# Optimization experiments

Hardware: AMD Instinct MI355X
Metric: run time of the kernel (lower is better)

## Reference

```python
import jax, jax.numpy as jnp
import numpy as np
import math

B, L, DM, H, ALPHA = 8, 2048, 512, 8, 3
DH = DM // H
SK = min(ALPHA * math.ceil(math.log(L)), L)    # sample_k = U_part = 24
NTOP = min(ALPHA * math.ceil(math.log(L)), L)  # n_top u = 24


def _ln(x, w, b, eps=1e-8):
    # TF-style layernorm (eps inside sqrt), matching custom LayerNorm
    u = x.mean(-1, keepdims=True)
    s = ((x - u) ** 2).mean(-1, keepdims=True)
    return w * (x - u) / jnp.sqrt(s + eps) + b


def setup_inputs() -> dict:
    key = jax.random.key(0)
    ks = jax.random.split(key, 12)
    p = lambda k, shape: jax.random.normal(k, shape, dtype=jnp.float32) * 0.02
    return {
        'queries': jax.random.normal(ks[0], (B, L, DM), dtype=jnp.float32),
        'keys': jax.random.normal(ks[1], (B, L, DM), dtype=jnp.float32),
        'values': jax.random.normal(ks[2], (B, L, DM), dtype=jnp.float32),
        'padding_mask': jnp.ones((B, L), dtype=jnp.float32),
        'Wq': p(ks[3], (DM, DM)), 'bq': jnp.zeros((DM,), jnp.float32),
        'Wk': p(ks[4], (DM, DM)), 'bk': jnp.zeros((DM,), jnp.float32),
        'Wv': p(ks[5], (DM, DM)), 'bv': jnp.zeros((DM,), jnp.float32),
        'Wf': p(ks[6], (DM, DM)), 'bf': jnp.zeros((DM,), jnp.float32),
        'qln_w': jnp.ones((DM,), jnp.float32), 'qln_b': jnp.zeros((DM,), jnp.float32),
        'fln_w': jnp.ones((DM,), jnp.float32), 'fln_b': jnp.zeros((DM,), jnp.float32),
        'index_sample': jax.random.randint(ks[7], (L, SK), 0, L, dtype=jnp.int32),
    }


def reference(queries, keys, values, padding_mask, Wq, bq, Wk, bk, Wv, bv, Wf, bf,
              qln_w, qln_b, fln_w, fln_b, index_sample):
    Bq, Lq, Dm = queries.shape
    Lk = keys.shape[1]
    Dh = Dm // H
    # projections + head split -> (B, H, L, Dh)
    q = (_ln(queries, qln_w, qln_b) @ Wq + bq).reshape(Bq, Lq, H, Dh).transpose(0, 2, 1, 3)
    k = (keys @ Wk + bk).reshape(Bq, Lk, H, Dh).transpose(0, 2, 1, 3)
    v = (values @ Wv + bv).reshape(Bq, Lk, H, Dh).transpose(0, 2, 1, 3)
    # _prob_QK: random K sampling + sparsity measure + top-n_top query selection
    K_sample = k[:, :, index_sample, :]                        # (B,H,Lq,SK,Dh) irregular gather
    QKs = jnp.einsum('bhid,bhijd->bhij', q, K_sample)          # (B,H,Lq,SK)
    M = QKs.max(-1) - QKs.sum(-1) / Lk
    _, m_top = jax.lax.top_k(M, NTOP)                          # (B,H,u)
    q_red = jnp.take_along_axis(q, m_top[..., None], axis=2)   # (B,H,u,Dh)
    # NOTE: source scales by 1/sqrt(full hidden dim D), not head size
    scores = jnp.einsum('bhud,bhkd->bhuk', q_red, k) * (1.0 / math.sqrt(Dm))
    # ProbMask: causal (key <= selected query pos) AND padding at selected queries
    causal = jnp.arange(Lk)[None, None, None, :] <= m_top[..., None]   # (B,H,u,Lk)
    pad_ind = padding_mask[jnp.arange(Bq)[:, None, None], m_top]       # (B,H,u)
    mask = causal & (pad_ind[..., None] != 0)
    scores = jnp.where(mask, scores, -100000.0)
    # initial values = causal cumulative mean of V (with_mask branch)
    v_avg = jnp.cumsum(v, axis=2) / (jnp.cumsum(padding_mask, -1)[:, None, :, None] + 1e-12)
    attn = jax.nn.softmax(scores, axis=-1)
    upd = jnp.einsum('bhuk,bhkd->bhud', attn, v)               # sparse attention output
    bi = jnp.arange(Bq)[:, None, None]
    hi = jnp.arange(H)[None, :, None]
    out = v_avg.at[bi, hi, m_top].set(upd)                     # scatter selected rows back
    out = out.transpose(0, 2, 1, 3).reshape(Bq, Lq, Dm)
    out = out @ Wf + bf
    return _ln(out, fln_w, fln_b)
```

## Files before the change

### kernel.cpp

```cpp
#include <hip/hip_runtime.h>
#include <math.h>

#define L 2048
#define DM 512
#define B_ 8
#define H_ 8
#define DH 64
#define SK 24
#define NTOP 24
#define CHUNK 128
#define NCH (L / CHUNK)
#define VC 32
#define VR 64
#define ABUF 4096

typedef __attribute__((ext_vector_type(8))) short short8;
typedef __attribute__((ext_vector_type(8))) __bf16 bf16x8;
typedef __attribute__((ext_vector_type(4))) float f32x4;

__device__ inline unsigned short f2bf(float x) {
    unsigned u = __float_as_uint(x);
    unsigned r = (u + 0x7FFFu + ((u >> 16) & 1u)) >> 16;
    return (unsigned short)r;
}
__device__ inline float bf2f(unsigned short h) {
    return __uint_as_float(((unsigned)h) << 16);
}

__device__ inline f32x4 MFMA_BF16(short8 a, short8 b, f32x4 c) {
    return __builtin_amdgcn_mfma_f32_16x16x32_bf16(
        __builtin_bit_cast(bf16x8, a), __builtin_bit_cast(bf16x8, b), c, 0, 0, 0);
}

template<bool WANTL>
__device__ inline void cvt8(const float4& x, const float4& y, short8& h, short8& l) {
    float v0 = x.x, v1 = x.y, v2 = x.z, v3 = x.w;
    float v4 = y.x, v5 = y.y, v6 = y.z, v7 = y.w;
    unsigned short h0 = f2bf(v0), h1 = f2bf(v1), h2 = f2bf(v2), h3 = f2bf(v3);
    unsigned short h4 = f2bf(v4), h5 = f2bf(v5), h6 = f2bf(v6), h7 = f2bf(v7);
    h[0] = (short)h0; h[1] = (short)h1; h[2] = (short)h2; h[3] = (short)h3;
    h[4] = (short)h4; h[5] = (short)h5; h[6] = (short)h6; h[7] = (short)h7;
    if (WANTL) {
        l[0] = (short)f2bf(v0 - bf2f(h0)); l[1] = (short)f2bf(v1 - bf2f(h1));
        l[2] = (short)f2bf(v2 - bf2f(h2)); l[3] = (short)f2bf(v3 - bf2f(h3));
        l[4] = (short)f2bf(v4 - bf2f(h4)); l[5] = (short)f2bf(v5 - bf2f(h5));
        l[6] = (short)f2bf(v6 - bf2f(h6)); l[7] = (short)f2bf(v7 - bf2f(h7));
    }
}

__device__ inline int lds_addr(int row, int kblk) {
    return row * 32 + ((kblk ^ ((row >> 1) & 3)) << 3);
}

__device__ inline float waveReduceSum(float v) {
    for (int o = 32; o > 0; o >>= 1) v += __shfl_down(v, o, 64);
    return v;
}
__device__ inline float waveReduceMax(float v) {
    for (int o = 32; o > 0; o >>= 1) v = fmaxf(v, __shfl_down(v, o, 64));
    return v;
}

__global__ __launch_bounds__(256)
void ln_kernel(const float* __restrict__ x, const float* __restrict__ w,
               const float* __restrict__ bvec, float* __restrict__ out) {
    int row = blockIdx.x;
    const float* xr = x + (size_t)row * DM;
    float* orow = out + (size_t)row * DM;
    int tid = threadIdx.x;
    float2 v = *(const float2*)(xr + tid * 2);
    float s = v.x + v.y;
    float sq = v.x * v.x + v.y * v.y;
    __shared__ float red[8];
    float ws = waveReduceSum(s);
    float wq = waveReduceSum(sq);
    int wid = tid >> 6, lane = tid & 63;
    if (lane == 0) { red[wid] = ws; red[4 + wid] = wq; }
    __syncthreads();
    float tot = red[0] + red[1] + red[2] + red[3];
    float totq = red[4] + red[5] + red[6] + red[7];
    float mean = tot * (1.0f / DM);
    float var = totq * (1.0f / DM) - mean * mean;
    float inv = rsqrtf(var + 1e-8f);
    float w0 = w[tid * 2], w1 = w[tid * 2 + 1];
    float b0 = bvec[tid * 2], b1 = bvec[tid * 2 + 1];
    float2 o;
    o.x = w0 * (v.x - mean) * inv + b0;
    o.y = w1 * (v.y - mean) * inv + b1;
    *(float2*)(orow + tid * 2) = o;
}

__global__ __launch_bounds__(256)
void ln_split_kernel(const float* __restrict__ x, const float* __restrict__ w,
                     const float* __restrict__ bvec,
                     unsigned short* __restrict__ oh, unsigned short* __restrict__ ol) {
    int row = blockIdx.x;
    const float* xr = x + (size_t)row * DM;
    int tid = threadIdx.x;
    float2 v = *(const float2*)(xr + tid * 2);
    float s = v.x + v.y;
    float sq = v.x * v.x + v.y * v.y;
    __shared__ float red[8];
    float ws = waveReduceSum(s);
    float wq = waveReduceSum(sq);
    int wid = tid >> 6, lane = tid & 63;
    if (lane == 0) { red[wid] = ws; red[4 + wid] = wq; }
    __syncthreads();
    float tot = red[0] + red[1] + red[2] + red[3];
    float totq = red[4] + red[5] + red[6] + red[7];
    float mean = tot * (1.0f / DM);
    float var = totq * (1.0f / DM) - mean * mean;
    float inv = rsqrtf(var + 1e-8f);
    float w0 = w[tid * 2], w1 = w[tid * 2 + 1];
    float b0 = bvec[tid * 2], b1 = bvec[tid * 2 + 1];
    float o0 = w0 * (v.x - mean) * inv + b0;
    float o1 = w1 * (v.y - mean) * inv + b1;
    ushort2 hh, ll;
    hh.x = f2bf(o0); ll.x = f2bf(o0 - bf2f(hh.x));
    hh.y = f2bf(o1); ll.y = f2bf(o1 - bf2f(hh.y));
    *(ushort2*)(oh + (size_t)row * DM + tid * 2) = hh;
    *(ushort2*)(ol + (size_t)row * DM + tid * 2) = ll;
}

__global__ __launch_bounds__(256)
void wsplit_kernel(const float* __restrict__ W, unsigned short* __restrict__ th,
                   unsigned short* __restrict__ tl) {
    __shared__ float ts[32][33];
    int k0 = blockIdx.y * 32, n0 = blockIdx.x * 32;
    int t = threadIdx.x;
    int r = t >> 3, c = (t & 7) * 4;
    float4 v = *(const float4*)(W + (size_t)(k0 + r) * 512 + n0 + c);
    ts[r][c] = v.x; ts[r][c + 1] = v.y; ts[r][c + 2] = v.z; ts[r][c + 3] = v.w;
    __syncthreads();
    float a0 = ts[c + 0][r], a1 = ts[c + 1][r], a2 = ts[c + 2][r], a3 = ts[c + 3][r];
    ushort4 h, l;
    h.x = f2bf(a0); l.x = f2bf(a0 - bf2f(h.x));
    h.y = f2bf(a1); l.y = f2bf(a1 - bf2f(h.y));
    h.z = f2bf(a2); l.z = f2bf(a2 - bf2f(h.z));
    h.w = f2bf(a3); l.w = f2bf(a3 - bf2f(h.w));
    *(ushort4*)(th + (size_t)(n0 + r) * 512 + k0 + c) = h;
    *(ushort4*)(tl + (size_t)(n0 + r) * 512 + k0 + c) = l;
}

template<int TERMS, int OMODE, int ACVT>
__device__ __forceinline__
void gemm_body(unsigned short* smem,
               const unsigned short* __restrict__ Ah, const unsigned short* __restrict__ Al,
               const float* __restrict__ Af,
               const unsigned short* __restrict__ Bh, const unsigned short* __restrict__ Bl,
               const float* __restrict__ bias, float* __restrict__ C,
               unsigned short* __restrict__ Ch, int orig) {
    unsigned short* sAh = smem;
    unsigned short* sAl = smem + ABUF;
    unsigned short* sBh = smem + (TERMS == 3 ? 2 : 1) * ABUF;
    unsigned short* sBl = sBh + ABUF;

    int j = (orig & 7) * 64 + (orig >> 3);
    int n0 = (j & 3) * 128, m0 = (j >> 2) * 128;

    int tid = threadIdx.x;
    int lane = tid & 63, wv = tid >> 6;
    int wr = wv >> 1, wc = wv & 1;
    int lrow = lane & 15, g = lane >> 4;

    int f0 = tid, f1 = tid + 256;
    int row0 = f0 >> 2, k0b = f0 & 3;
    int row1 = f1 >> 2, k1b = f1 & 3;
    int sa0 = lds_addr(row0, k0b), sa1 = lds_addr(row1, k1b);
    int c0 = k0b * 8, c1 = k1b * 8;

    f32x4 acc[4][4];
#pragma unroll
    for (int mf = 0; mf < 4; mf++)
#pragma unroll
        for (int nf = 0; nf < 4; nf++) acc[mf][nf] = (f32x4){0.f, 0.f, 0.f, 0.f};

    short8 rAh0, rAh1, rAl0, rAl1, rBh0, rBh1, rBl0, rBl1;
    float4 fA00, fA01, fA10, fA11;

    auto LOAD = [&](int kt) {
        int k0 = kt * 32;
        if (ACVT) {
            fA00 = *(const float4*)(Af + (size_t)(m0 + row0) * 512 + k0 + c0);
            fA01 = *(const float4*)(Af + (size_t)(m0 + row0) * 512 + k0 + c0 + 4);
            fA10 = *(const float4*)(Af + (size_t)(m0 + row1) * 512 + k0 + c1);
            fA11 = *(const float4*)(Af + (size_t)(m0 + row1) * 512 + k0 + c1 + 4);
        } else {
            rAh0 = *(const short8*)(Ah + (size_t)(m0 + row0) * 512 + k0 + c0);
            rAh1 = *(const short8*)(Ah + (size_t)(m0 + row1) * 512 + k0 + c1);
            if (TERMS == 3) {
                rAl0 = *(const short8*)(Al + (size_t)(m0 + row0) * 512 + k0 + c0);
                rAl1 = *(const short8*)(Al + (size_t)(m0 + row1) * 512 + k0 + c1);
            }
        }
        rBh0 = *(const short8*)(Bh + (size_t)(n0 + row0) * 512 + k0 + c0);
        rBh1 = *(const short8*)(Bh + (size_t)(n0 + row1) * 512 + k0 + c1);
        if (TERMS >= 2) {
            rBl0 = *(const short8*)(Bl + (size_t)(n0 + row0) * 512 + k0 + c0);
            rBl1 = *(const short8*)(Bl + (size_t)(n0 + row1) * 512 + k0 + c1);
        }
    };
    auto STORE = [&]() {
        if (ACVT) {
            cvt8<TERMS == 3>(fA00, fA01, rAh0, rAl0);
            cvt8<TERMS == 3>(fA10, fA11, rAh1, rAl1);
        }
        *(short8*)&sAh[sa0] = rAh0;
        *(short8*)&sAh[sa1] = rAh1;
        if (TERMS == 3) {
            *(short8*)&sAl[sa0] = rAl0;
            *(short8*)&sAl[sa1] = rAl1;
        }
        *(short8*)&sBh[sa0] = rBh0;
        *(short8*)&sBh[sa1] = rBh1;
        if (TERMS >= 2) {
            *(short8*)&sBl[sa0] = rBl0;
            *(short8*)&sBl[sa1] = rBl1;
        }
    };

    int ra = wr * 64 + lrow;
    int rb = wc * 64 + lrow;
    int abase = ra * 32 + ((g ^ ((ra >> 1) & 3)) << 3);
    int bbase = rb * 32 + ((g ^ ((rb >> 1) & 3)) << 3);

    LOAD(0);
    for (int kt = 0; kt < 16; kt++) {
        STORE();
        __syncthreads();
        if (kt < 15) LOAD(kt + 1);
        short8 ah[4], al[4], bh[4], bl[4];
#pragma unroll
        for (int mf = 0; mf < 4; mf++) {
            ah[mf] = *(const short8*)&sAh[abase + mf * 512];
            if (TERMS == 3) al[mf] = *(const short8*)&sAl[abase + mf * 512];
        }
#pragma unroll
        for (int nf = 0; nf < 4; nf++) {
            bh[nf] = *(const short8*)&sBh[bbase + nf * 512];
            if (TERMS >= 2) bl[nf] = *(const short8*)&sBl[bbase + nf * 512];
        }
#pragma unroll
        for (int mf = 0; mf < 4; mf++)
#pragma unroll
            for (int nf = 0; nf < 4; nf++) {
                acc[mf][nf] = MFMA_BF16(ah[mf], bh[nf], acc[mf][nf]);
                if (TERMS >= 2) acc[mf][nf] = MFMA_BF16(ah[mf], bl[nf], acc[mf][nf]);
                if (TERMS == 3) acc[mf][nf] = MFMA_BF16(al[mf], bh[nf], acc[mf][nf]);
            }
        __syncthreads();
    }

    int crow0 = m0 + wr * 64 + (lane >> 4) * 4;
    int ccol0 = n0 + wc * 64 + lrow;
    float bb[4];
#pragma unroll
    for (int nf = 0; nf < 4; nf++) bb[nf] = bias[ccol0 + nf * 16];
#pragma unroll
    for (int mf = 0; mf < 4; mf++)
#pragma unroll
        for (int nf = 0; nf < 4; nf++)
#pragma unroll
            for (int r = 0; r < 4; r++) {
                float val = acc[mf][nf][r] + bb[nf];
                size_t idx = (size_t)(crow0 + mf * 16 + r) * 512 + ccol0 + nf * 16;
                if (OMODE != 2) C[idx] = val;
                if (OMODE != 0) Ch[idx] = f2bf(val);
            }
}

__global__ __launch_bounds__(256, 2)
void qkv_gemm(const unsigned short* __restrict__ lnq_h, const unsigned short* __restrict__ lnq_l,
              const float* __restrict__ keys, const float* __restrict__ values,
              const unsigned short* __restrict__ wq_h, const unsigned short* __restrict__ wq_l,
              const unsigned short* __restrict__ wk_h, const unsigned short* __restrict__ wk_l,
              const unsigned short* __restrict__ wv_h, const unsigned short* __restrict__ wv_l,
              const float* __restrict__ bq, const float* __restrict__ bk, const float* __restrict__ bv,
              float* __restrict__ qb, float* __restrict__ kb,
              unsigned short* __restrict__ kb_h, unsigned short* __restrict__ vb_h) {
    __shared__ __align__(16) unsigned short smem[4 * ABUF];
    int orig = blockIdx.x + 4 * blockIdx.y;
    if (blockIdx.z == 0)
        gemm_body<3, 0, 0>(smem, lnq_h, lnq_l, nullptr, wq_h, wq_l, bq, qb, nullptr, orig);
    else if (blockIdx.z == 1)
        gemm_body<3, 1, 1>(smem, nullptr, nullptr, keys, wk_h, wk_l, bk, kb, kb_h, orig);
    else
        gemm_body<1, 2, 1>(smem, nullptr, nullptr, values, wv_h, wv_l, bv, nullptr, vb_h, orig);
}

template<int TERMS, int OMODE, int ACVT>
__global__ __launch_bounds__(256, 2)
void gemm_mfma(const unsigned short* __restrict__ Ah, const unsigned short* __restrict__ Al,
               const float* __restrict__ Af,
               const unsigned short* __restrict__ Bh, const unsigned short* __restrict__ Bl,
               const float* __restrict__ bias, float* __restrict__ C,
               unsigned short* __restrict__ Ch) {
    __shared__ __align__(16) unsigned short smem[(TERMS == 3 ? 4 : (TERMS == 2 ? 3 : 2)) * ABUF];
    int orig = blockIdx.x + 4 * blockIdx.y;
    gemm_body<TERMS, OMODE, ACVT>(smem, Ah, Al, Af, Bh, Bl, bias, C, Ch, orig);
}

__global__ __launch_bounds__(256)
void sample_m_kernel(const float* __restrict__ q, const float* __restrict__ k,
                     const int* __restrict__ idx, float* __restrict__ M) {
    int bid = blockIdx.x;
    int b = bid & 7;
    int ig = bid >> 3;
    int wv = threadIdx.x >> 6, lane = threadIdx.x & 63;
    int i = ig * 4 + wv;
    const float* qrow = q + ((size_t)b * L + i) * DM + lane * 8;
    float4 q0 = *(const float4*)qrow;
    float4 q1 = *(const float4*)(qrow + 4);
    int myidx = 0;
    if (lane < SK) myidx = idx[i * SK + lane];
    float sj[SK];
#pragma unroll
    for (int j = 0; j < SK; j++) {
        int row = __shfl(myidx, j, 64);
        const float* kp = k + ((size_t)b * L + row) * DM + lane * 8;
        float4 k0 = *(const float4*)kp;
        float4 k1 = *(const float4*)(kp + 4);
        sj[j] = q0.x * k0.x + q0.y * k0.y + q0.z * k0.z + q0.w * k0.w
              + q1.x * k1.x + q1.y * k1.y + q1.z * k1.z + q1.w * k1.w;
    }
    float mx = -1e30f, sm = 0.f;
#pragma unroll
    for (int j = 0; j < SK; j++) {
        float s = sj[j];
        s += __shfl_xor(s, 1, 64);
        s += __shfl_xor(s, 2, 64);
        s += __shfl_xor(s, 4, 64);
        mx = fmaxf(mx, s);
        sm += s;
    }
    if ((lane & 7) == 0) {
        int h = lane >> 3;
        M[((size_t)b * H_ + h) * L + i] = mx - sm * (1.0f / L);
    }
}

__global__ __launch_bounds__(64)
void topk_kernel(const float* __restrict__ M, int* __restrict__ mtop) {
    int bh = blockIdx.x;
    int lane = threadIdx.x;
    const float* Mr = M + (size_t)bh * L;
    float m[32];
#pragma unroll
    for (int r = 0; r < 32; r++) m[r] = Mr[r * 64 + lane];
    for (int it = 0; it < NTOP; it++) {
        float bv = -1e30f; int br = 0;
#pragma unroll
        for (int r = 0; r < 32; r++) {
            bool better = m[r] > bv;
            br = better ? r : br;
            bv = better ? m[r] : bv;
        }
        int bt = (br << 6) | lane;
#pragma unroll
        for (int o = 1; o < 64; o <<= 1) {
            float ov = __shfl_xor(bv, o, 64);
            int ot = __shfl_xor(bt, o, 64);
            bool take = (ov > bv) || (ov == bv && ot < bt);
            bv = take ? ov : bv;
            bt = take ? ot : bt;
        }
        if (lane == 0) mtop[bh * NTOP + it] = bt;
        int rwin = bt >> 6;
        bool mine = (bt & 63) == lane;
#pragma unroll
        for (int r = 0; r < 32; r++)
            if (mine && (r == rwin)) m[r] = -1e30f;
    }
}

__global__ __launch_bounds__(256)
void qprep_kernel(const float* __restrict__ qb, const int* __restrict__ mtop,
                  const float* __restrict__ pad, unsigned short* __restrict__ qsel,
                  int* __restrict__ lim_arr) {
    int bh = blockIdx.x; int b = bh >> 3, h = bh & 7;
    int tid = threadIdx.x;
#pragma unroll
    for (int l = 0; l < 2; l++) {
        int f = tid + l * 256;
        int u = f >> 4, seg = (f & 15) * 4;
        ushort4 o;
        if (u < NTOP) {
            int iq = mtop[bh * NTOP + u];
            bool ok = pad[(size_t)b * L + iq] != 0.f;
            float sc = ok ? 0.044194173824159216f : 0.f;
            float4 qv = *(const float4*)(qb + ((size_t)b * L + iq) * DM + h * DH + seg);
            o.x = f2bf(qv.x * sc); o.y = f2bf(qv.y * sc);
            o.z = f2bf(qv.z * sc); o.w = f2bf(qv.w * sc);
            if (seg == 0) lim_arr[bh * 32 + u] = ok ? iq : (L - 1);
        } else {
            o.x = o.y = o.z = o.w = 0;
            if (seg == 0) lim_arr[bh * 32 + u] = -1;
        }
        *(ushort4*)(qsel + ((size_t)bh * 32 + u) * 64 + seg) = o;
    }
}

__global__ __launch_bounds__(256)
void padscan_kernel(const float* __restrict__ pad, float* __restrict__ denom) {
    int b = blockIdx.x;
    __shared__ float tot[256];
    int tid = threadIdx.x;
    const float* p = pad + (size_t)b * L;
    float loc[8];
    float s = 0.f;
#pragma unroll
    for (int u = 0; u < 8; u++) { s += p[tid * 8 + u]; loc[u] = s; }
    tot[tid] = s;
    __syncthreads();
    for (int off = 1; off < 256; off <<= 1) {
        float add = (tid >= off) ? tot[tid - off] : 0.f;
        __syncthreads();
        tot[tid] += add;
        __syncthreads();
    }
    float excl = tot[tid] - s;
#pragma unroll
    for (int u = 0; u < 8; u++) denom[(size_t)b * L + tid * 8 + u] = excl + loc[u];
}

__global__ __launch_bounds__(256)
void vsum_kernel(const unsigned short* __restrict__ vh, float* __restrict__ csum) {
    int c = blockIdx.x, b = blockIdx.y;
    int d2 = threadIdx.x;
    size_t base = ((size_t)b * L + c * VR) * DM + d2 * 2;
    float a0 = 0.f, a1 = 0.f;
    for (int t = 0; t < VR; t++) {
        unsigned v = *(const unsigned*)(vh + base + (size_t)t * DM);
        a0 += bf2f((unsigned short)(v & 0xffff));
        a1 += bf2f((unsigned short)(v >> 16));
    }
    float2 st = {a0, a1};
    *(float2*)(csum + ((size_t)b * VC + c) * DM + d2 * 2) = st;
}

__global__ __launch_bounds__(256)
void vavg_kernel(const unsigned short* __restrict__ vh, const float* __restrict__ csum,
                 const float* __restrict__ denom, unsigned short* __restrict__ out_h) {
    int c = blockIdx.x, b = blockIdx.y;
    int d2 = threadIdx.x;
    float a0 = 0.f, a1 = 0.f;
    for (int cc = 0; cc < c; cc++) {
        float2 t = *(const float2*)(csum + ((size_t)b * VC + cc) * DM + d2 * 2);
        a0 += t.x; a1 += t.y;
    }
    size_t base = ((size_t)b * L + c * VR) * DM + d2 * 2;
    for (int t = 0; t < VR; t++) {
        unsigned v = *(const unsigned*)(vh + base + (size_t)t * DM);
        a0 += bf2f((unsigned short)(v & 0xffff));
        a1 += bf2f((unsigned short)(v >> 16));
        float dn = denom[(size_t)b * L + c * VR + t] + 1e-12f;
        unsigned o = (unsigned)f2bf(a0 / dn) | ((unsigned)f2bf(a1 / dn) << 16);
        *(unsigned*)(out_h + base + (size_t)t * DM) = o;
    }
}

__global__ __launch_bounds__(256)
void attn_chunk_mfma(const unsigned short* __restrict__ kbh,
                     const unsigned short* __restrict__ vbh,
                     const unsigned short* __restrict__ qsel,
                     const int* __restrict__ lim_arr,
                     float* __restrict__ part_m, float* __restrict__ part_s,
                     float* __restrict__ part_acc) {
    int c = blockIdx.x, bh = blockIdx.y;
    int b = bh >> 3, h = bh & 7;
    int j0 = c * CHUNK;
    __shared__ __align__(16) unsigned short KV[128 * 64];
    __shared__ __align__(16) unsigned short Ps[32 * 128];
    __shared__ __align__(16) unsigned short Qs[32 * 64];
    __shared__ float redm[4][32];
    __shared__ float reds[4][32];
    __shared__ int lims[32];

    int tid = threadIdx.x;
    int wv = tid >> 6, lane = tid & 63;
    int l15 = lane & 15, g = lane >> 4;

    const unsigned short* kpanel = kbh + ((size_t)b * L + j0) * DM + h * DH;
    short8 kreg[4];
#pragma unroll
    for (int l = 0; l < 4; l++) {
        int f = tid + l * 256;
        int jr = f >> 3, blk = f & 7;
        kreg[l] = *(const short8*)(kpanel + (size_t)jr * DM + blk * 8);
    }
    {
        int u = tid >> 3, blk = tid & 7;
        short8 qreg = *(const short8*)(qsel + ((size_t)bh * 32 + u) * 64 + blk * 8);
        *(short8*)&Qs[u * 64 + (((blk ^ (u & 7))) << 3)] = qreg;
    }
#pragma unroll
    for (int l = 0; l < 4; l++) {
        int f = tid + l * 256;
        int jr = f >> 3, blk = f & 7;
        *(short8*)&KV[jr * 64 + ((blk ^ (jr & 7)) << 3)] = kreg[l];
    }
    if (tid < 32) lims[tid] = lim_arr[bh * 32 + tid];
    __syncthreads();

    f32x4 sf[2][2];
#pragma unroll
    for (int mf = 0; mf < 2; mf++)
#pragma unroll
        for (int nf = 0; nf < 2; nf++) sf[mf][nf] = (f32x4){0.f, 0.f, 0.f, 0.f};
#pragma unroll
    for (int ks = 0; ks < 2; ks++) {
        short8 aq[2], bk[2];
#pragma unroll
        for (int mf = 0; mf < 2; mf++) {
            int u = mf * 16 + l15;
            int blk = (ks * 4 + g) ^ (u & 7);
            aq[mf] = *(const short8*)&Qs[u * 64 + (blk << 3)];
        }
#pragma unroll
        for (int nf = 0; nf < 2; nf++) {
            int jr = wv * 32 + nf * 16 + l15;
            int blk = (ks * 4 + g) ^ (jr & 7);
            bk[nf] = *(const short8*)&KV[jr * 64 + (blk << 3)];
        }
#pragma unroll
        for (int mf = 0; mf < 2; mf++)
#pragma unroll
            for (int nf = 0; nf < 2; nf++)
                sf[mf][nf] = MFMA_BF16(aq[mf], bk[nf], sf[mf][nf]);
    }

    const unsigned short* vpanel = vbh + ((size_t)b * L + j0) * DM + h * DH;
    short8 vreg[4];
#pragma unroll
    for (int l = 0; l < 4; l++) {
        int f = tid + l * 256;
        int jr = f >> 3, blk = f & 7;
        vreg[l] = *(const short8*)(vpanel + (size_t)jr * DM + blk * 8);
    }

    float sv[2][2][4];
    float mx[2][4];
#pragma unroll
    for (int mf = 0; mf < 2; mf++)
#pragma unroll
        for (int r = 0; r < 4; r++) {
            int u = mf * 16 + g * 4 + r;
            int limv = lims[u];
            float m = -1e30f;
#pragma unroll
            for (int nf = 0; nf < 2; nf++) {
                int jg = j0 + wv * 32 + nf * 16 + l15;
                float s = (jg <= limv) ? sf[mf][nf][r] : -1e30f;
                sv[mf][nf][r] = s;
                m = fmaxf(m, s);
            }
            m = fmaxf(m, __shfl_xor(m, 1, 64));
            m = fmaxf(m, __shfl_xor(m, 2, 64));
            m = fmaxf(m, __shfl_xor(m, 4, 64));
            m = fmaxf(m, __shfl_xor(m, 8, 64));
            mx[mf][r] = m;
        }
    if (l15 == 0) {
#pragma unroll
        for (int mf = 0; mf < 2; mf++)
#pragma unroll
            for (int r = 0; r < 4; r++)
                redm[wv][mf * 16 + g * 4 + r] = mx[mf][r];
    }
    __syncthreads();

    float lmax[2][4], smv[2][4];
#pragma unroll
    for (int mf = 0; mf < 2; mf++)
#pragma unroll
        for (int r = 0; r < 4; r++) {
            int u = mf * 16 + g * 4 + r;
            float m = fmaxf(fmaxf(redm[0][u], redm[1][u]),
                            fmaxf(redm[2][u], redm[3][u]));
            lmax[mf][r] = m;
            bool any = m > -1e29f;
            float sm = 0.f;
#pragma unroll
            for (int nf = 0; nf < 2; nf++) {
                float e = any ? __expf(sv[mf][nf][r] - m) : 0.f;
                sm += e;
                int jr = wv * 32 + nf * 16 + l15;
                Ps[u * 128 + (((jr >> 3) ^ (u & 7)) << 3) + (jr & 7)] = f2bf(e);
            }
            sm += __shfl_xor(sm, 1, 64);
            sm += __shfl_xor(sm, 2, 64);
            sm += __shfl_xor(sm, 4, 64);
            sm += __shfl_xor(sm, 8, 64);
            smv[mf][r] = sm;
        }
    if (l15 == 0) {
#pragma unroll
        for (int mf = 0; mf < 2; mf++)
#pragma unroll
            for (int r = 0; r < 4; r++)
                reds[wv][mf * 16 + g * 4 + r] = smv[mf][r];
    }
#pragma unroll
    for (int l = 0; l < 4; l++) {
        int f = tid + l * 256;
        int jr = f >> 3, blk = f & 7;
        short8 w = vreg[l];
        if ((jr >> 3) & 1) w = __builtin_shufflevector(w, w, 4, 5, 6, 7, 0, 1, 2, 3);
        *(short8*)&KV[jr * 64 + ((blk ^ (jr & 7)) << 3)] = w;
    }
    __syncthreads();

    if (wv == 0 && l15 == 0) {
#pragma unroll
        for (int mf = 0; mf < 2; mf++)
#pragma unroll
            for (int r = 0; r < 4; r++) {
                int u = mf * 16 + g * 4 + r;
                if (u < NTOP) {
                    float ss = reds[0][u] + reds[1][u] + reds[2][u] + reds[3][u];
                    part_m[(bh * NTOP + u) * NCH + c] = lmax[mf][r];
                    part_s[(bh * NTOP + u) * NCH + c] = ss;
                }
            }
    }

    f32x4 of[2];
    of[0] = (f32x4){0.f, 0.f, 0.f, 0.f};
    of[1] = (f32x4){0.f, 0.f, 0.f, 0.f};
    int d = wv * 16 + l15;
#pragma unroll
    for (int ks = 0; ks < 4; ks++) {
        unsigned short va[8];
#pragma unroll
        for (int i = 0; i < 8; i++) {
            int jr = ks * 32 + g * 8 + i;
            int addr = jr * 64 + (((d >> 3) ^ (jr & 7)) << 3)
                     + ((d & 7) ^ (((jr >> 3) & 1) << 2));
            va[i] = KV[addr];
        }
        short8 av;
#pragma unroll
        for (int i = 0; i < 8; i++) av[i] = (short)va[i];
        short8 bp[2];
#pragma unroll
        for (int nf = 0; nf < 2; nf++) {
            int u = nf * 16 + l15;
            int blk = (ks * 4 + g) ^ (u & 7);
            bp[nf] = *(const short8*)&Ps[u * 128 + (blk << 3)];
        }
#pragma unroll
        for (int nf = 0; nf < 2; nf++)
            of[nf] = MFMA_BF16(av, bp[nf], of[nf]);
    }
#pragma unroll
    for (int nf = 0; nf < 2; nf++) {
        int u = nf * 16 + l15;
        if (u < NTOP) {
#pragma unroll
            for (int r = 0; r < 4; r++)
                part_acc[((size_t)(bh * NTOP + u) * NCH + c) * 64 + wv * 16 + g * 4 + r] =
                    of[nf][r];
        }
    }
}

__global__ __launch_bounds__(256)
void attn_merge_kernel(const float* __restrict__ part_m, const float* __restrict__ part_s,
                       const float* __restrict__ part_acc, const int* __restrict__ mtop,
                       unsigned short* __restrict__ pre_h) {
    int ug = blockIdx.x;
    int bh = blockIdx.y;
    int b = bh >> 3, h = bh & 7;
    int tid = threadIdx.x;
    int u = ug * 4 + (tid >> 6);
    int d = tid & 63;
    int base = (bh * NTOP + u) * NCH;
    float m = -1e30f;
#pragma unroll
    for (int c = 0; c < NCH; c++) m = fmaxf(m, part_m[base + c]);
    float s = 0.f, o = 0.f;
#pragma unroll
    for (int c = 0; c < NCH; c++) {
        float w = __expf(part_m[base + c] - m);
        s += part_s[base + c] * w;
        o = fmaf(part_acc[(size_t)(base + c) * 64 + d], w, o);
    }
    o /= s;
    int iq = mtop[bh * NTOP + u];
    pre_h[((size_t)b * L + iq) * DM + h * DH + d] = f2bf(o);
}

extern "C" void kernel_launch(void* const* d_in, const int* in_sizes, int n_in,
                              void* d_out, int out_size, void* d_ws, size_t ws_size,
                              hipStream_t stream) {
    const float* queries = (const float*)d_in[0];
    const float* keys    = (const float*)d_in[1];
    const float* values  = (const float*)d_in[2];
    const float* pad     = (const float*)d_in[3];
    const float* Wq = (const float*)d_in[4];  const float* bq = (const float*)d_in[5];
    const float* Wk = (const float*)d_in[6];  const float* bk = (const float*)d_in[7];
    const float* Wv = (const float*)d_in[8];  const float* bv = (const float*)d_in[9];
    const float* Wf = (const float*)d_in[10]; const float* bfv = (const float*)d_in[11];
    const float* qlnw = (const float*)d_in[12]; const float* qlnb = (const float*)d_in[13];
    const float* flnw = (const float*)d_in[14]; const float* flnb = (const float*)d_in[15];
    const int* idx = (const int*)d_in[16];

    float* ws = (float*)d_ws;
    const size_t NE = (size_t)B_ * L * DM;
    float* qb    = ws;
    float* kb    = ws + NE;
    unsigned short* vb_h = (unsigned short*)(ws + 2 * NE);
    unsigned short* kb_h = vb_h + NE;
    unsigned short* qsel = (unsigned short*)(ws + 3 * NE);
    int* lim_arr = (int*)(qsel + 64 * 32 * 64);
    float* Mbuf  = ws + 4 * NE;
    float* denom = Mbuf + (size_t)B_ * H_ * L;
    float* csum  = denom + (size_t)B_ * L;
    int*   mtop  = (int*)(csum + (size_t)B_ * VC * DM);
    unsigned short* bfr = (unsigned short*)(mtop + 2048);
    unsigned short* pre_h = bfr;
    unsigned short* wts   = bfr + NE;
    unsigned short* wq_h = wts;              unsigned short* wq_l = wts + 262144;
    unsigned short* wk_h = wts + 2 * 262144; unsigned short* wk_l = wts + 3 * 262144;
    unsigned short* wv_h = wts + 4 * 262144; unsigned short* wv_l = wts + 5 * 262144;
    unsigned short* wf_h = wts + 6 * 262144; unsigned short* wf_l = wts + 7 * 262144;

    float* tmp = (float*)d_out;
    unsigned short* lnq_h = (unsigned short*)d_out;
    unsigned short* lnq_l = lnq_h + NE;
    float* part_m   = tmp;
    float* part_s   = part_m + 64 * NTOP * NCH;
    float* part_acc = part_s + 64 * NTOP * NCH;

    padscan_kernel<<<B_, 256, 0, stream>>>(pad, denom);
    ln_split_kernel<<<B_ * L, 256, 0, stream>>>(queries, qlnw, qlnb, lnq_h, lnq_l);
    dim3 gw(16, 16);
    wsplit_kernel<<<gw, 256, 0, stream>>>(Wq, wq_h, wq_l);
    wsplit_kernel<<<gw, 256, 0, stream>>>(Wk, wk_h, wk_l);
    wsplit_kernel<<<gw, 256, 0, stream>>>(Wv, wv_h, wv_l);
    wsplit_kernel<<<gw, 256, 0, stream>>>(Wf, wf_h, wf_l);

    dim3 gq(4, 128, 3);
    qkv_gemm<<<gq, 256, 0, stream>>>(lnq_h, lnq_l, keys, values,
                                     wq_h, wq_l, wk_h, wk_l, wv_h, wv_l,
                                     bq, bk, bv, qb, kb, kb_h, vb_h);

    sample_m_kernel<<<B_ * L / 4, 256, 0, stream>>>(qb, kb, idx, Mbuf);
    topk_kernel<<<B_ * H_, 64, 0, stream>>>(Mbuf, mtop);
    qprep_kernel<<<64, 256, 0, stream>>>(qb, mtop, pad, qsel, lim_arr);
    dim3 gv(VC, B_);
    vsum_kernel<<<gv, 256, 0, stream>>>(vb_h, csum);
    vavg_kernel<<<gv, 256, 0, stream>>>(vb_h, csum, denom, pre_h);
    dim3 gc(NCH, 64);
    attn_chunk_mfma<<<gc, 256, 0, stream>>>(kb_h, vb_h, qsel, lim_arr,
                                            part_m, part_s, part_acc);
    dim3 gmg(6, 64);
    attn_merge_kernel<<<gmg, 256, 0, stream>>>(part_m, part_s, part_acc, mtop, pre_h);
    dim3 gg(4, 128);
    gemm_mfma<1, 0, 0><<<gg, 256, 0, stream>>>(pre_h, nullptr, nullptr, wf_h, wf_l, bfv, (float*)d_out, nullptr);
    ln_kernel<<<B_ * L, 256, 0, stream>>>((float*)d_out, flnw, flnb, (float*)d_out);
}
```

Before: 242.3 us.

## Load GEMM B tiles directly into LDS with double buffering

Moves the B-operand (weight) tile loads from a register staging path to global_load_lds direct-to-LDS transfers. The B tiles are double-buffered so the next tile streams in while the current one is consumed, and the XOR swizzle is applied on the source address. This cuts register pressure and the VGPR-to-LDS store instructions, at the cost of more LDS per block. The larger LDS footprint may reduce occupancy, and the asynchronous loads depend on correct waitcnt/barrier ordering.

New measurement: 254.8 us. +5.2%, slower.

```diff
diff --git a/kernel.cpp b/kernel.cpp
--- a/kernel.cpp
+++ b/kernel.cpp
@@ -30,6 +30,12 @@
 __device__ inline f32x4 MFMA_BF16(short8 a, short8 b, f32x4 c) {
     return __builtin_amdgcn_mfma_f32_16x16x32_bf16(
         __builtin_bit_cast(bf16x8, a), __builtin_bit_cast(bf16x8, b), c, 0, 0, 0);
+}
+
+__device__ __forceinline__ void gload16(const unsigned short* g, unsigned short* l) {
+    __builtin_amdgcn_global_load_lds(
+        (const __attribute__((address_space(1))) void*)g,
+        (__attribute__((address_space(3))) void*)l, 16, 0, 0);
 }
 
 template<bool WANTL>
@@ -150,10 +156,11 @@
                const unsigned short* __restrict__ Bh, const unsigned short* __restrict__ Bl,
                const float* __restrict__ bias, float* __restrict__ C,
                unsigned short* __restrict__ Ch, int orig) {
+    constexpr int A_ARR = (TERMS == 3) ? 2 : 1;
+    constexpr int B_ARR = (TERMS >= 2) ? 2 : 1;
     unsigned short* sAh = smem;
     unsigned short* sAl = smem + ABUF;
-    unsigned short* sBh = smem + (TERMS == 3 ? 2 : 1) * ABUF;
-    unsigned short* sBl = sBh + ABUF;
+    unsigned short* sB  = smem + A_ARR * ABUF;
 
     int j = (orig & 7) * 64 + (orig >> 3);
     int n0 = (j & 3) * 128, m0 = (j >> 2) * 128;
@@ -163,11 +170,10 @@
     int wr = wv >> 1, wc = wv & 1;
     int lrow = lane & 15, g = lane >> 4;
 
-    int f0 = tid, f1 = tid + 256;
-    int row0 = f0 >> 2, k0b = f0 & 3;
-    int row1 = f1 >> 2, k1b = f1 & 3;
-    int sa0 = lds_addr(row0, k0b), sa1 = lds_addr(row1, k1b);
-    int c0 = k0b * 8, c1 = k1b * 8;
+    int row0 = tid >> 2, k0b = tid & 3;
+    int row1 = row0 + 64;
+    int sa0 = lds_addr(row0, k0b), sa1 = lds_addr(row1, k0b);
+    int c0 = k0b * 8;
 
     f32x4 acc[4][4];
 #pragma unroll
@@ -175,32 +181,26 @@
 #pragma unroll
         for (int nf = 0; nf < 4; nf++) acc[mf][nf] = (f32x4){0.f, 0.f, 0.f, 0.f};
 
-    short8 rAh0, rAh1, rAl0, rAl1, rBh0, rBh1, rBl0, rBl1;
+    short8 rAh0, rAh1, rAl0, rAl1;
     float4 fA00, fA01, fA10, fA11;
 
-    auto LOAD = [&](int kt) {
+    auto LOAD_A = [&](int kt) {
         int k0 = kt * 32;
         if (ACVT) {
             fA00 = *(const float4*)(Af + (size_t)(m0 + row0) * 512 + k0 + c0);
             fA01 = *(const float4*)(Af + (size_t)(m0 + row0) * 512 + k0 + c0 + 4);
-            fA10 = *(const float4*)(Af + (size_t)(m0 + row1) * 512 + k0 + c1);
-            fA11 = *(const float4*)(Af + (size_t)(m0 + row1) * 512 + k0 + c1 + 4);
+            fA10 = *(const float4*)(Af + (size_t)(m0 + row1) * 512 + k0 + c0);
+            fA11 = *(const float4*)(Af + (size_t)(m0 + row1) * 512 + k0 + c0 + 4);
         } else {
             rAh0 = *(const short8*)(Ah + (size_t)(m0 + row0) * 512 + k0 + c0);
-            rAh1 = *(const short8*)(Ah + (size_t)(m0 + row1) * 512 + k0 + c1);
+            rAh1 = *(const short8*)(Ah + (size_t)(m0 + row1) * 512 + k0 + c0);
             if (TERMS == 3) {
                 rAl0 = *(const short8*)(Al + (size_t)(m0 + row0) * 512 + k0 + c0);
-                rAl1 = *(const short8*)(Al + (size_t)(m0 + row1) * 512 + k0 + c1);
+                rAl1 = *(const short8*)(Al + (size_t)(m0 + row1) * 512 + k0 + c0);
             }
         }
-        rBh0 = *(const short8*)(Bh + (size_t)(n0 + row0) * 512 + k0 + c0);
-        rBh1 = *(const short8*)(Bh + (size_t)(n0 + row1) * 512 + k0 + c1);
-        if (TERMS >= 2) {
-            rBl0 = *(const short8*)(Bl + (size_t)(n0 + row0) * 512 + k0 + c0);
-            rBl1 = *(const short8*)(Bl + (size_t)(n0 + row1) * 512 + k0 + c1);
-        }
     };
-    auto STORE = [&]() {
+    auto STORE_A = [&]() {
         if (ACVT) {
             cvt8<TERMS == 3>(fA00, fA01, rAh0, rAl0);
             cvt8<TERMS == 3>(fA10, fA11, rAh1, rAl1);
@@ -211,11 +211,21 @@
             *(short8*)&sAl[sa0] = rAl0;
             *(short8*)&sAl[sa1] = rAl1;
         }
-        *(short8*)&sBh[sa0] = rBh0;
-        *(short8*)&sBh[sa1] = rBh1;
+    };
+    auto GLOAD_B = [&](int kt, int buf) {
+        int k0 = kt * 32;
+        int r0 = wv * 16 + (lane >> 2);
+        int kpos = lane & 3;
+        int src0 = (kpos ^ ((r0 >> 1) & 3)) * 8;
+        int r1 = r0 + 64;
+        int src1 = (kpos ^ ((r1 >> 1) & 3)) * 8;
+        unsigned short* bh = sB + (buf * B_ARR + 0) * ABUF;
+        gload16(Bh + (size_t)(n0 + r0) * 512 + k0 + src0, bh + wv * 512);
+        gload16(Bh + (size_t)(n0 + r1) * 512 + k0 + src1, bh + 2048 + wv * 512);
         if (TERMS >= 2) {
-            *(short8*)&sBl[sa0] = rBl0;
-            *(short8*)&sBl[sa1] = rBl1;
+            unsigned short* bl = sB + (buf * B_ARR + 1) * ABUF;
+            gload16(Bl + (size_t)(n0 + r0) * 512 + k0 + src0, bl + wv * 512);
+            gload16(Bl + (size_t)(n0 + r1) * 512 + k0 + src1, bl + 2048 + wv * 512);
         }
     };
 
@@ -224,11 +234,14 @@
     int abase = ra * 32 + ((g ^ ((ra >> 1) & 3)) << 3);
     int bbase = rb * 32 + ((g ^ ((rb >> 1) & 3)) << 3);
 
-    LOAD(0);
+    LOAD_A(0);
+    GLOAD_B(0, 0);
     for (int kt = 0; kt < 16; kt++) {
-        STORE();
+        STORE_A();
         __syncthreads();
-        if (kt < 15) LOAD(kt + 1);
+        if (kt < 15) { GLOAD_B(kt + 1, (kt + 1) & 1); LOAD_A(kt + 1); }
+        const unsigned short* bhB = sB + ((kt & 1) * B_ARR + 0) * ABUF;
+        const unsigned short* blB = sB + ((kt & 1) * B_ARR + 1) * ABUF;
         short8 ah[4], al[4], bh[4], bl[4];
 #pragma unroll
         for (int mf = 0; mf < 4; mf++) {
@@ -237,8 +250,8 @@
         }
 #pragma unroll
         for (int nf = 0; nf < 4; nf++) {
-            bh[nf] = *(const short8*)&sBh[bbase + nf * 512];
-            if (TERMS >= 2) bl[nf] = *(const short8*)&sBl[bbase + nf * 512];
+            bh[nf] = *(const short8*)&bhB[bbase + nf * 512];
+            if (TERMS >= 2) bl[nf] = *(const short8*)&blB[bbase + nf * 512];
         }
 #pragma unroll
         for (int mf = 0; mf < 4; mf++)
@@ -278,7 +291,7 @@
               const float* __restrict__ bq, const float* __restrict__ bk, const float* __restrict__ bv,
               float* __restrict__ qb, float* __restrict__ kb,
               unsigned short* __restrict__ kb_h, unsigned short* __restrict__ vb_h) {
-    __shared__ __align__(16) unsigned short smem[4 * ABUF];
+    __shared__ __align__(16) unsigned short smem[6 * ABUF];
     int orig = blockIdx.x + 4 * blockIdx.y;
     if (blockIdx.z == 0)
         gemm_body<3, 0, 0>(smem, lnq_h, lnq_l, nullptr, wq_h, wq_l, bq, qb, nullptr, orig);
@@ -295,7 +308,8 @@
                const unsigned short* __restrict__ Bh, const unsigned short* __restrict__ Bl,
                const float* __restrict__ bias, float* __restrict__ C,
                unsigned short* __restrict__ Ch) {
-    __shared__ __align__(16) unsigned short smem[(TERMS == 3 ? 4 : (TERMS == 2 ? 3 : 2)) * ABUF];
+    constexpr int NB = ((TERMS == 3) ? 2 : 1) + ((TERMS >= 2) ? 4 : 2);
+    __shared__ __align__(16) unsigned short smem[NB * ABUF];
     int orig = blockIdx.x + 4 * blockIdx.y;
     gemm_body<TERMS, OMODE, ACVT>(smem, Ah, Al, Af, Bh, Bl, bias, C, Ch, orig);
 }
```
